# Kernel optimization log

Hardware: AMD Instinct MI355X
Metric: run time of the kernel (lower is better)

Reference implementation:

```python
import jax, jax.numpy as jnp
import numpy as np

B, S, DIM = 2, 2048, 2048
NH, NKV = 16, 16
HD = 128            # constructor head_dim (full per-head dim, = 2 * self.head_dim)
HHD = HD // 2       # self.head_dim = per-stream dim = 64
ROPE_THETA = 10000.0
LAMBDA_INIT = 0.8 - 0.6 * float(np.exp(-0.3 * 0))  # block_id = 0 -> 0.2
EPS = 1e-5


def make_freq_cis(seq_len, dim, theta):
    # rotation matrices, shape (seq, dim//2, 2, 2): [[cos, -sin], [sin, cos]]
    inv = 1.0 / (theta ** (np.arange(0, dim, 2, dtype=np.float32) / dim))
    ang = np.arange(seq_len, dtype=np.float32)[:, None] * inv[None, :]
    cos, sin = np.cos(ang), np.sin(ang)
    fc = np.stack([np.stack([cos, -sin], -1), np.stack([sin, cos], -1)], -2)
    return jnp.asarray(fc, dtype=jnp.float32)


def setup_inputs() -> dict:
    key = jax.random.key(0)
    ks = jax.random.split(key, 9)
    std = DIM ** -0.5
    return {
        "x": jax.random.normal(ks[0], (B, S, DIM), jnp.float32),
        "freq_cis": make_freq_cis(S, HD, ROPE_THETA),
        "wq": jax.random.normal(ks[1], (NH * HD, DIM), jnp.float32) * std,
        "wk": jax.random.normal(ks[2], (NKV * HD, DIM), jnp.float32) * std,
        "wv": jax.random.normal(ks[3], (NKV * HD, DIM), jnp.float32) * std,
        "wo": jax.random.normal(ks[4], (DIM, NH * HD), jnp.float32) * std,
        "lambda_q1": jax.random.normal(ks[5], (HHD,), jnp.float32) * 0.1,
        "lambda_k1": jax.random.normal(ks[6], (HHD,), jnp.float32) * 0.1,
        "lambda_q2": jax.random.normal(ks[7], (HHD,), jnp.float32) * 0.1,
        "lambda_k2": jax.random.normal(ks[8], (HHD,), jnp.float32) * 0.1,
        "subln_w": jnp.ones((HD,), jnp.float32),
    }


def _rope(t, fc):
    # t: (b, s, h, d); fc: (s, d//2, 2, 2). Pairs (even, odd) rotated by 2x2 matrix.
    b, s, h, d = t.shape
    t2 = t.reshape(b, s, h, d // 2, 1, 2)
    out = (t2 * fc[None, :, None]).sum(-1)  # (b, s, h, d//2, 2)
    return out.reshape(b, s, h, d)


def _causal_attn(q, k, v):
    # q, k: (b, s, h, HHD); v: (b, s, h, HD). Flash-attn default scale = 1/sqrt(q head dim).
    scale = 1.0 / jnp.sqrt(jnp.asarray(q.shape[-1], q.dtype))
    scores = jnp.einsum('bqhd,bkhd->bhqk', q, k) * scale
    s = q.shape[1]
    causal = jnp.tril(jnp.ones((s, s), bool))
    scores = jnp.where(causal, scores, jnp.finfo(scores.dtype).min)
    p = jax.nn.softmax(scores, axis=-1)
    return jnp.einsum('bhqk,bkhd->bqhd', p, v)  # (b, s, h, HD)


def reference(x, freq_cis, wq, wk, wv, wo, lambda_q1, lambda_k1, lambda_q2, lambda_k2, subln_w):
    b, s, _ = x.shape
    xq = (x @ wq.T).reshape(b, s, NH, HD)
    xk = (x @ wk.T).reshape(b, s, NKV, HD)
    xv = (x @ wv.T).reshape(b, s, NKV, HD)
    xq = _rope(xq, freq_cis)
    xk = _rope(xk, freq_cis)
    if NKV != NH:  # GQA: repeat kv heads group-wise
        rep = NH // NKV
        xk = jnp.repeat(xk, rep, axis=2)
        xv = jnp.repeat(xv, rep, axis=2)
    # split each head into two differential streams of size HHD
    xq = xq.reshape(b, s, NH, 2, HHD)
    xk = xk.reshape(b, s, NH, 2, HHD)
    attn1 = _causal_attn(xq[:, :, :, 0], xk[:, :, :, 0], xv)
    attn2 = _causal_attn(xq[:, :, :, 1], xk[:, :, :, 1], xv)
    lam1 = jnp.exp(jnp.sum(lambda_q1 * lambda_k1))
    lam2 = jnp.exp(jnp.sum(lambda_q2 * lambda_k2))
    lam_full = lam1 - lam2 + LAMBDA_INIT
    attn = attn1 - lam_full * attn2              # (b, s, h, HD)
    attn = jnp.transpose(attn, (0, 2, 1, 3))     # faithful to torch .transpose(1, 2)
    ms = jnp.mean(jnp.square(attn), axis=-1, keepdims=True)
    attn = attn * jax.lax.rsqrt(ms + EPS) * subln_w  # RMSNorm(2*HHD)
    attn = attn * (1.0 - LAMBDA_INIT)
    # faithful to original: reshape (b, h, s, HD) row-major into (b, s, h*HD)
    attn = attn.reshape(b, s, NH * HD)
    return attn @ wo.T
```

## Files before the change

kernel.cpp:

```cpp
#include <hip/hip_runtime.h>

typedef unsigned short u16;
typedef unsigned int   u32;
typedef __attribute__((ext_vector_type(8))) short s16x8;
typedef __attribute__((ext_vector_type(4))) float f32x4;
typedef __attribute__((ext_vector_type(4))) u32   u32x4;

constexpr int Bc = 2, Sc = 2048, DIMc = 2048, NHc = 16, HDc = 128, Tc = Bc * Sc;
constexpr float LAMBDA_INIT_C = 0.2f;

__device__ __forceinline__ u16 f2bf(float f) {
  union { float f; u32 u; } v; v.f = f;
  u32 r = v.u + 0x7fffu + ((v.u >> 16) & 1u);
  return (u16)(r >> 16);
}
__device__ __forceinline__ float bf2f(u16 b) {
  union { u32 u; float f; } v; v.u = ((u32)b) << 16;
  return v.f;
}
__device__ __forceinline__ f32x4 mfma16(s16x8 a, s16x8 b, f32x4 c) {
  return __builtin_amdgcn_mfma_f32_16x16x32_bf16(a, b, c, 0, 0, 0);
}

typedef const __attribute__((address_space(1))) u32 gq32;
typedef __attribute__((address_space(3))) u32 lq32;
__device__ __forceinline__ void cp16(const u16* g, u16* l) {
  __builtin_amdgcn_global_load_lds((gq32*)g, (lq32*)l, 16, 0, 0);
}

#define BAR()    asm volatile("s_barrier" ::: "memory")
#define LGKM(n)  asm volatile("s_waitcnt lgkmcnt(" #n ")" ::: "memory")
#define VMC(n)   asm volatile("s_waitcnt vmcnt(" #n ")" ::: "memory")
#define SCHED0() __builtin_amdgcn_sched_barrier(0)

__global__ void cvt_all_kernel(const float* __restrict__ x,
                               const float* __restrict__ wq, const float* __restrict__ wk,
                               const float* __restrict__ wv, const float* __restrict__ wo,
                               u16* __restrict__ xb, u16* __restrict__ wb) {
  const int i = blockIdx.x * 256 + threadIdx.x;
  constexpr int NX = Tc * DIMc / 4;
  constexpr int PW = DIMc * DIMc / 4;
  float4 v; uint2* dst;
  if (i < NX) {
    v = ((const float4*)x)[i];
    dst = ((uint2*)xb) + i;
  } else {
    const int j = i - NX;
    const int which = j >> 20;
    const int jj = j & (PW - 1);
    const float* src = which == 0 ? wq : which == 1 ? wk : which == 2 ? wv : wo;
    v = ((const float4*)src)[jj];
    dst = ((uint2*)wb) + j;
  }
  union { u16 u[4]; uint2 p; } o;
  o.u[0] = f2bf(v.x); o.u[1] = f2bf(v.y); o.u[2] = f2bf(v.z); o.u[3] = f2bf(v.w);
  *dst = o.p;
}

__global__ __launch_bounds__(512, 2) void gemm8p(const u16* __restrict__ A,
                                                 const u16* __restrict__ Bw,
                                                 u16* __restrict__ Cb) {
  constexpr int K = 2048, NT = K / 64;
  constexpr int AU = 128 * 64;
  constexpr int BU = 256 * 64;
  __shared__ __align__(16) u16 L[2 * AU + 3 * BU];

  const int tid  = threadIdx.x;
  const int lane = tid & 63, w = tid >> 6;
  const int wm = w >> 2, wn = w & 3;
  const int l15 = lane & 15, quad = lane >> 4;

  const int mt   = gridDim.y;
  const int nwg  = gridDim.x * mt;
  const int flat = blockIdx.x * mt + blockIdx.y;
  const int swz  = (flat & 7) * (nwg >> 3) + (flat >> 3);
  const int nbase = (swz / mt) * 256;
  const int mbase = (swz % mt) * 128;

  const u16* Ag = A  + (size_t)mbase * K;
  const u16* Bg = Bw + (size_t)nbase * K;

  u32 soffA[2], dlinA[2], soffB[4], dlinB[4];
#pragma unroll
  for (int l = 0; l < 2; l++) {
    const int n = l * 512 + tid;
    const int r = n >> 3;
    const u32 q = (u32)((n & 7) ^ (r & 7));
    soffA[l] = (u32)r * K + q * 8;
    dlinA[l] = (u32)n * 8;
  }
#pragma unroll
  for (int l = 0; l < 4; l++) {
    const int n = l * 512 + tid;
    const int r = n >> 3;
    const u32 q = (u32)((n & 7) ^ (r & 7));
    soffB[l] = (u32)r * K + q * 8;
    dlinB[l] = (u32)n * 8;
  }

  auto stA = [&](int kt, int ab) {
    u16* base = L + ab * AU;
#pragma unroll
    for (int l = 0; l < 2; l++)
      cp16(Ag + (size_t)kt * 64 + soffA[l], base + dlinA[l]);
  };
  auto stB = [&](int kt, int bb) {
    u16* base = L + 2 * AU + bb * BU;
#pragma unroll
    for (int l = 0; l < 4; l++)
      cp16(Bg + (size_t)kt * 64 + soffB[l], base + dlinB[l]);
  };

  const int aB  = (wm * 64 + l15) * 64;
  const int bB  = (wn * 64 + l15) * 64;
  const int xq0 = (quad ^ (l15 & 7)) << 3;

  f32x4 acc[4][4];
#pragma unroll
  for (int i = 0; i < 4; i++)
#pragma unroll
    for (int j = 0; j < 4; j++) acc[i][j] = (f32x4){0.f, 0.f, 0.f, 0.f};

  stB(0, 0); stA(0, 0); stB(1, 1);
  VMC(4);
  BAR();

  s16x8 a0[4], b0[4], a1[4], b1[4];
  int abR = 0, bbR = 0;

  for (int kt = 0; kt < NT; ++kt) {
    const int tgA = (kt + 1 < NT) ? kt + 1 : 0;
    const int tgB = (kt + 2 < NT) ? kt + 2 : 0;
    const int abW = abR ^ 1;
    const int bbW = (bbR + 2 >= 3) ? bbR - 1 : bbR + 2;

    const u16* Ab = L + abR * AU;
    const u16* Bb = L + 2 * AU + bbR * BU;

#pragma unroll
    for (int j = 0; j < 4; j++)
      b0[j] = *(const s16x8*)(Bb + bB + j * 1024 + xq0);
#pragma unroll
    for (int i = 0; i < 4; i++)
      a0[i] = *(const s16x8*)(Ab + aB + i * 1024 + xq0);
    SCHED0();
#pragma unroll
    for (int j = 0; j < 4; j++)
      b1[j] = *(const s16x8*)(Bb + bB + j * 1024 + (xq0 ^ 32));
#pragma unroll
    for (int i = 0; i < 4; i++)
      a1[i] = *(const s16x8*)(Ab + aB + i * 1024 + (xq0 ^ 32));
    SCHED0();
    stA(tgA, abW);
    stB(tgB, bbW);

    LGKM(8); SCHED0();
    __builtin_amdgcn_s_setprio(1);
#pragma unroll
    for (int i = 0; i < 4; i++)
#pragma unroll
      for (int j = 0; j < 4; j++) acc[i][j] = mfma16(a0[i], b0[j], acc[i][j]);
    __builtin_amdgcn_s_setprio(0);

    LGKM(0); SCHED0();
    __builtin_amdgcn_s_setprio(1);
#pragma unroll
    for (int i = 0; i < 4; i++)
#pragma unroll
      for (int j = 0; j < 4; j++) acc[i][j] = mfma16(a1[i], b1[j], acc[i][j]);
    __builtin_amdgcn_s_setprio(0);

    VMC(4);
    BAR();

    abR = abW;
    bbR = (bbR + 1 == 3) ? 0 : bbR + 1;
  }
  asm volatile("s_waitcnt vmcnt(0)" ::: "memory");

  const int which = nbase >> 11;
  const int ncol  = nbase & 2047;
  u16* Ob = Cb + (size_t)which * ((size_t)Tc * DIMc);
#pragma unroll
  for (int i = 0; i < 4; i++) {
    const int m0 = mbase + wm * 64 + i * 16 + quad * 4;
#pragma unroll
    for (int j = 0; j < 4; j++) {
      const int n0 = ncol + wn * 64 + j * 16 + l15;
#pragma unroll
      for (int r = 0; r < 4; r++)
        Ob[(size_t)(m0 + r) * 2048 + n0] = f2bf(acc[i][j][r]);
    }
  }
}

__global__ __launch_bounds__(256, 2) void gemm128o(const u16* __restrict__ A,
                                                   const u16* __restrict__ Bw,
                                                   float* __restrict__ Cf) {
  constexpr int K = 2048, NT = K / 64;
  constexpr int AU = 128 * 64;
  constexpr int BU = 128 * 64;
  __shared__ __align__(16) u16 L[2 * AU + 3 * BU];

  const int tid  = threadIdx.x;
  const int lane = tid & 63, w = tid >> 6;
  const int wm = w >> 1, wn = w & 1;
  const int l15 = lane & 15, quad = lane >> 4;

  const int mt   = gridDim.y;
  const int nwg  = gridDim.x * mt;
  const int flat = blockIdx.x * mt + blockIdx.y;
  const int swz  = (flat & 7) * (nwg >> 3) + (flat >> 3);
  const int nbase = (swz / mt) * 128;
  const int mbase = (swz % mt) * 128;

  const u16* Ag = A  + (size_t)mbase * K;
  const u16* Bg = Bw + (size_t)nbase * K;

  u32 soff[4], dlin[4];
#pragma unroll
  for (int l = 0; l < 4; l++) {
    const int n = l * 256 + tid;
    const int r = n >> 3;
    const u32 q = (u32)((n & 7) ^ (r & 7));
    soff[l] = (u32)r * K + q * 8;
    dlin[l] = (u32)n * 8;
  }

  auto stA = [&](int kt, int ab) {
    u16* base = L + ab * AU;
#pragma unroll
    for (int l = 0; l < 4; l++)
      cp16(Ag + (size_t)kt * 64 + soff[l], base + dlin[l]);
  };
  auto stB = [&](int kt, int bb) {
    u16* base = L + 2 * AU + bb * BU;
#pragma unroll
    for (int l = 0; l < 4; l++)
      cp16(Bg + (size_t)kt * 64 + soff[l], base + dlin[l]);
  };

  const int aB  = (wm * 64 + l15) * 64;
  const int bB  = (wn * 64 + l15) * 64;
  const int xq0 = (quad ^ (l15 & 7)) << 3;

  f32x4 acc[4][4];
#pragma unroll
  for (int i = 0; i < 4; i++)
#pragma unroll
    for (int j = 0; j < 4; j++) acc[i][j] = (f32x4){0.f, 0.f, 0.f, 0.f};

  stB(0, 0); stA(0, 0); stB(1, 1);
  VMC(4);
  BAR();

  s16x8 a0[4], b0[4], a1[4], b1[4];
  int abR = 0, bbR = 0;

  for (int kt = 0; kt < NT; ++kt) {
    const int tgA = (kt + 1 < NT) ? kt + 1 : 0;
    const int tgB = (kt + 2 < NT) ? kt + 2 : 0;
    const int abW = abR ^ 1;
    const int bbW = (bbR + 2 >= 3) ? bbR - 1 : bbR + 2;

    const u16* Ab = L + abR * AU;
    const u16* Bb = L + 2 * AU + bbR * BU;

#pragma unroll
    for (int j = 0; j < 4; j++)
      b0[j] = *(const s16x8*)(Bb + bB + j * 1024 + xq0);
#pragma unroll
    for (int i = 0; i < 4; i++)
      a0[i] = *(const s16x8*)(Ab + aB + i * 1024 + xq0);
    SCHED0();
#pragma unroll
    for (int j = 0; j < 4; j++)
      b1[j] = *(const s16x8*)(Bb + bB + j * 1024 + (xq0 ^ 32));
#pragma unroll
    for (int i = 0; i < 4; i++)
      a1[i] = *(const s16x8*)(Ab + aB + i * 1024 + (xq0 ^ 32));
    SCHED0();
    stA(tgA, abW);
    stB(tgB, bbW);

    LGKM(8); SCHED0();
    __builtin_amdgcn_s_setprio(1);
#pragma unroll
    for (int i = 0; i < 4; i++)
#pragma unroll
      for (int j = 0; j < 4; j++) acc[i][j] = mfma16(a0[i], b0[j], acc[i][j]);
    __builtin_amdgcn_s_setprio(0);

    LGKM(0); SCHED0();
    __builtin_amdgcn_s_setprio(1);
#pragma unroll
    for (int i = 0; i < 4; i++)
#pragma unroll
      for (int j = 0; j < 4; j++) acc[i][j] = mfma16(a1[i], b1[j], acc[i][j]);
    __builtin_amdgcn_s_setprio(0);

    VMC(4);
    BAR();

    abR = abW;
    bbR = (bbR + 1 == 3) ? 0 : bbR + 1;
  }
  asm volatile("s_waitcnt vmcnt(0)" ::: "memory");

#pragma unroll
  for (int i = 0; i < 4; i++) {
    const int m0 = mbase + wm * 64 + i * 16 + quad * 4;
#pragma unroll
    for (int j = 0; j < 4; j++) {
      const int n0 = nbase + wn * 64 + j * 16 + l15;
#pragma unroll
      for (int r = 0; r < 4; r++)
        Cf[(size_t)(m0 + r) * 2048 + n0] = acc[i][j][r];
    }
  }
}

__global__ void prep_kernel(const u16* __restrict__ qg, const u16* __restrict__ kg,
                            const u16* __restrict__ vg, const float* __restrict__ fc,
                            u16* __restrict__ qr, u16* __restrict__ kr,
                            u16* __restrict__ vt) {
  __shared__ u16 tile[64][33];
  const int bid = blockIdx.x;
  if (bid < 8192) {
    const bool isq = bid < 4096;
    const u16* xg = isq ? qg : kg;
    u16* outp = isq ? qr : kr;
    const float scale = isq ? 0.125f : 1.0f;
    const int idx = (bid & 4095) * 256 + threadIdx.x;
    const int p4 = idx & 15;
    const int hh = (idx >> 4) & 15;
    const int tt = idx >> 8;
    const int s  = tt & (Sc - 1);
    const int bb = tt >> 11;
    const u32x4 xp = *(const u32x4*)(xg + (size_t)tt * DIMc + hh * HDc + p4 * 8);
    u32x4 ow;
#pragma unroll
    for (int pp = 0; pp < 4; pp++) {
      const int p = p4 * 4 + pp;
      const float4 f = ((const float4*)fc)[s * 64 + p];
      const float c = f.x * scale, sn = f.z * scale;
      const u32 wd = xp[pp];
      const float x0 = bf2f((u16)wd), x1 = bf2f((u16)(wd >> 16));
      ow[pp] = (u32)f2bf(c * x0 - sn * x1) | ((u32)f2bf(sn * x0 + c * x1) << 16);
    }
    *(u32x4*)(outp + ((size_t)(bb * NHc + hh) * Sc + s) * HDc + p4 * 8) = ow;
  } else {
    const int vb = bid - 8192;
    const int bh = vb >> 7;
    const int bb = bh >> 4, hh = bh & 15;
    const int rem = vb & 127;
    const int s0 = (rem & 63) * 32, d0 = (rem >> 6) * 64;
    const int tx = threadIdx.x & 31, ty = threadIdx.x >> 5;
#pragma unroll
    for (int pp = 0; pp < 4; pp++) {
      const int s = s0 + ty + pp * 8;
      const u32 v = *(const u32*)(vg + (size_t)(bb * Sc + s) * DIMc + hh * HDc + d0 + tx * 2);
      tile[tx * 2][ty + pp * 8]     = (u16)v;
      tile[tx * 2 + 1][ty + pp * 8] = (u16)(v >> 16);
    }
    __syncthreads();
    const int dr = threadIdx.x >> 4;
    const int sx = threadIdx.x & 15;
#pragma unroll
    for (int pp = 0; pp < 4; pp++) {
      const int d = dr + pp * 16;
      const u32 wd = (u32)tile[d][sx * 2] | ((u32)tile[d][sx * 2 + 1] << 16);
      *(u32*)(vt + ((size_t)bh * HDc + d0 + d) * Sc + s0 + sx * 2) = wd;
    }
  }
}

__global__ __launch_bounds__(256, 3) void diff_attn_kernel(
    const u16* __restrict__ qr, const u16* __restrict__ kr, const u16* __restrict__ vt,
    const float* __restrict__ lq1, const float* __restrict__ lk1,
    const float* __restrict__ lq2, const float* __restrict__ lk2,
    const float* __restrict__ subw, u16* __restrict__ Y) {
  __shared__ u16 KB[2][8192];
  __shared__ u16 VB[2][8192];

  const int h = blockIdx.y, b = blockIdx.z;
  const int t = 31 - (int)blockIdx.x;
  const int bh = b * NHc + h;
  const int tid = threadIdx.x;
  const int w = tid >> 6, lane = tid & 63;
  const int l15 = lane & 15, quad = lane >> 4;

  const u16* krb = kr + (size_t)bh * Sc * HDc;
  const u16* vtb = vt + (size_t)bh * HDc * Sc;

  float lp1 = lq1[lane] * lk1[lane];
  float lp2 = lq2[lane] * lk2[lane];
#pragma unroll
  for (int m = 32; m; m >>= 1) { lp1 += __shfl_xor(lp1, m); lp2 += __shfl_xor(lp2, m); }
  const float lam = __expf(lp1) - __expf(lp2) + LAMBDA_INIT_C;

  float wsub[8];
#pragma unroll
  for (int dn = 0; dn < 8; dn++) wsub[dn] = subw[dn * 16 + l15];

  u32 offK[4], offV[4], dstO[4];
#pragma unroll
  for (int oo = 0; oo < 4; oo++) {
    const int n = w * 256 + oo * 64 + lane;
    const int s = n & 31, dblk = (n >> 5) & 15, sub = n >> 9;
    const int mkey = (s & 3) + ((s >> 2) & 3) * 8 + ((s >> 4) << 2);
    offK[oo] = (u32)((sub * 32 + mkey) * HDc + dblk * 8);
    offV[oo] = (u32)((n & 127) * Sc + (sub * 32 + ((n >> 7) & 3) * 8));
    dstO[oo] = (u32)(n * 8);
  }

  const int rowbase = t * 64 + w * 16;
  const int nc = t + 1;

  const u16* qp = qr + ((size_t)bh * Sc + rowbase + l15) * HDc + quad * 8;
  s16x8 qa[2][2];
  qa[0][0] = *(const s16x8*)(qp);
  qa[0][1] = *(const s16x8*)(qp + 32);
  qa[1][0] = *(const s16x8*)(qp + 64);
  qa[1][1] = *(const s16x8*)(qp + 96);

  f32x4 o[2][8];
#pragma unroll
  for (int st = 0; st < 2; st++)
#pragma unroll
    for (int dn = 0; dn < 8; dn++) o[st][dn] = (f32x4){0.f, 0.f, 0.f, 0.f};
  float lpart[2] = { 0.f, 0.f };

#pragma unroll
  for (int oo = 0; oo < 4; oo++) cp16(krb + offK[oo], KB[0] + dstO[oo]);
#pragma unroll
  for (int oo = 0; oo < 4; oo++) cp16(vtb + offV[oo], VB[0] + dstO[oo]);

  for (int c = 0; c < nc; c++) {
    __syncthreads();
    if (c + 1 < nc) {
      const int kb1 = (c + 1) * 64;
      u16* Kn = KB[(c + 1) & 1];
      u16* Vn = VB[(c + 1) & 1];
#pragma unroll
      for (int oo = 0; oo < 4; oo++) cp16(krb + (size_t)kb1 * HDc + offK[oo], Kn + dstO[oo]);
#pragma unroll
      for (int oo = 0; oo < 4; oo++) cp16(vtb + offV[oo] + kb1, Vn + dstO[oo]);
    }
    const u16* Kb = KB[c & 1];
    const u16* Vb = VB[c & 1];
    const int kb = c * 64;
    const bool diag = (c == nc - 1);

#pragma unroll
    for (int sub = 0; sub < 2; sub++) {
      if (diag && sub == 1 && w < 2) continue;

      f32x4 sc[2][2];
#pragma unroll
      for (int st = 0; st < 2; st++)
#pragma unroll
        for (int kt = 0; kt < 2; kt++) sc[st][kt] = (f32x4){0.f, 0.f, 0.f, 0.f};
#pragma unroll
      for (int st = 0; st < 2; st++)
#pragma unroll
        for (int kh = 0; kh < 2; kh++) {
          const int base = sub * 512 + (st * 8 + kh * 4 + quad) * 32;
#pragma unroll
          for (int kt = 0; kt < 2; kt++) {
            const s16x8 kf = *(const s16x8*)(Kb + (size_t)(base + kt * 16 + l15) * 8);
            sc[st][kt] = mfma16(kf, qa[st][kh], sc[st][kt]);
          }
        }

      s16x8 pa[2];
#pragma unroll
      for (int st = 0; st < 2; st++) {
        float p[8];
#pragma unroll
        for (int kt = 0; kt < 2; kt++)
#pragma unroll
          for (int r = 0; r < 4; r++) p[kt * 4 + r] = __expf(sc[st][kt][r]);
        if (diag) {
          const int qrow = rowbase + l15;
          const int kb0 = kb + sub * 32 + quad * 8;
#pragma unroll
          for (int j8 = 0; j8 < 8; j8++)
            if (kb0 + j8 > qrow) p[j8] = 0.f;
        }
        float sm = 0.f;
#pragma unroll
        for (int j8 = 0; j8 < 8; j8++) sm += p[j8];
        lpart[st] += sm;
        union { u16 us[8]; s16x8 vv; } pk;
#pragma unroll
        for (int j8 = 0; j8 < 8; j8++) pk.us[j8] = f2bf(p[j8]);
        pa[st] = pk.vv;
      }

#pragma unroll
      for (int dn = 0; dn < 8; dn++) {
        const s16x8 vf =
            *(const s16x8*)(Vb + (size_t)(sub * 512 + quad * 128 + dn * 16 + l15) * 8);
        o[0][dn] = mfma16(pa[0], vf, o[0][dn]);
        o[1][dn] = mfma16(pa[1], vf, o[1][dn]);
      }
    }
  }

  float lL0 = lpart[0], lL1 = lpart[1];
  lL0 += __shfl_xor(lL0, 16); lL0 += __shfl_xor(lL0, 32);
  lL1 += __shfl_xor(lL1, 16); lL1 += __shfl_xor(lL1, 32);
  const float inv1 = 1.f / lL0;
  const float inv2 = lam / lL1;
  float i1C[4], i2C[4];
#pragma unroll
  for (int r = 0; r < 4; r++) {
    i1C[r] = __shfl(inv1, quad * 4 + r, 16);
    i2C[r] = __shfl(inv2, quad * 4 + r, 16);
  }
  float yv[8][4], ss[4] = { 0.f, 0.f, 0.f, 0.f };
#pragma unroll
  for (int dn = 0; dn < 8; dn++)
#pragma unroll
    for (int r = 0; r < 4; r++) {
      const float y = o[0][dn][r] * i1C[r] - o[1][dn][r] * i2C[r];
      yv[dn][r] = y;
      ss[r] += y * y;
    }
#pragma unroll
  for (int r = 0; r < 4; r++) {
#pragma unroll
    for (int mm = 1; mm < 16; mm <<= 1) ss[r] += __shfl_xor(ss[r], mm);
  }
  float scl[4];
#pragma unroll
  for (int r = 0; r < 4; r++) scl[r] = rsqrtf(ss[r] * (1.f / 128.f) + 1e-5f) * 0.8f;

  u16* yrow = Y + ((size_t)(b * Sc + h * 128 + t * 4 + w)) * 2048;
#pragma unroll
  for (int dn = 0; dn < 8; dn++)
#pragma unroll
    for (int r = 0; r < 4; r++)
      yrow[(quad * 4 + r) * 128 + dn * 16 + l15] = f2bf(yv[dn][r] * scl[r] * wsub[dn]);
}

extern "C" void kernel_launch(void* const* d_in, const int* in_sizes, int n_in,
                              void* d_out, int out_size, void* d_ws, size_t ws_size,
                              hipStream_t stream) {
  const float* x    = (const float*)d_in[0];
  const float* fc   = (const float*)d_in[1];
  const float* wq   = (const float*)d_in[2];
  const float* wk   = (const float*)d_in[3];
  const float* wv   = (const float*)d_in[4];
  const float* wo   = (const float*)d_in[5];
  const float* lq1  = (const float*)d_in[6];
  const float* lk1  = (const float*)d_in[7];
  const float* lq2  = (const float*)d_in[8];
  const float* lk2  = (const float*)d_in[9];
  const float* subw = (const float*)d_in[10];
  float* out = (float*)d_out;

  char* ws = (char*)d_ws;
  constexpr size_t SZ_X  = (size_t)Tc * DIMc * 2;
  constexpr size_t SZ_W  = (size_t)DIMc * DIMc * 2;
  constexpr size_t SZ_T  = (size_t)Tc * DIMc * 2;
  u16* xb  = (u16*)(ws);
  u16* wqb = (u16*)(ws + SZ_X);
  u16* wob = (u16*)(ws + SZ_X + 3 * SZ_W);
  u16* qg  = (u16*)(ws + SZ_X + 4 * SZ_W);
  u16* kg  = (u16*)(ws + SZ_X + 4 * SZ_W + SZ_T);
  u16* vg  = (u16*)(ws + SZ_X + 4 * SZ_W + 2 * SZ_T);
  u16* qr  = (u16*)(ws + SZ_X + 4 * SZ_W + 3 * SZ_T);
  u16* kr  = (u16*)(ws + SZ_X + 4 * SZ_W + 4 * SZ_T);
  u16* vt  = (u16*)(ws + SZ_X + 4 * SZ_W + 5 * SZ_T);
  u16* Y   = (u16*)(ws + SZ_X + 4 * SZ_W + 6 * SZ_T);

  cvt_all_kernel<<<(Tc * DIMc / 4 + 4 * DIMc * DIMc / 4) / 256, 256, 0, stream>>>(
      x, wq, wk, wv, wo, xb, wqb);

  gemm8p<<<dim3(DIMc * 3 / 256, Tc / 128), 512, 0, stream>>>(xb, wqb, qg);

  prep_kernel<<<8192 + 4096, 256, 0, stream>>>(qg, kg, vg, fc, qr, kr, vt);

  diff_attn_kernel<<<dim3(32, NHc, Bc), 256, 0, stream>>>(
      qr, kr, vt, lq1, lk1, lq2, lk2, subw, Y);

  gemm128o<<<dim3(DIMc / 128, Tc / 128), 256, 0, stream>>>(Y, wob, out);
}
```

Before: 505.0 us.

## Merge two adjacent query tiles per 512-thread block sharing K/V loads

Each attention block now has 8 waves covering two consecutive 64-row query tiles, so every K/V chunk copied into shared memory serves 128 query rows and global/LDS load traffic per row is halved. Each thread issues half as many async copies per chunk. The lower tile's waves skip the last chunk but still hit the barriers, which leaves some idle wave time. The order of query tiles alternates by batch and block parity to balance causal work across the grid. Launch bounds change to 512 threads, which tightens the register budget per wave.

```diff
diff --git a/kernel.cpp b/kernel.cpp
--- a/kernel.cpp
+++ b/kernel.cpp
@@ -375,7 +375,7 @@
   }
 }
 
-__global__ __launch_bounds__(256, 3) void diff_attn_kernel(
+__global__ __launch_bounds__(512, 4) void diff_attn_kernel(
     const u16* __restrict__ qr, const u16* __restrict__ kr, const u16* __restrict__ vt,
     const float* __restrict__ lq1, const float* __restrict__ lk1,
     const float* __restrict__ lq2, const float* __restrict__ lk2,
@@ -384,12 +384,17 @@
   __shared__ u16 VB[2][8192];
 
   const int h = blockIdx.y, b = blockIdx.z;
-  const int t = 31 - (int)blockIdx.x;
+  const int bx = blockIdx.x;
+  const int uu = ((bx & 1) ^ b) ? (bx >> 1) : 15 - (bx >> 1);
   const int bh = b * NHc + h;
   const int tid = threadIdx.x;
   const int w = tid >> 6, lane = tid & 63;
   const int l15 = lane & 15, quad = lane >> 4;
 
+  const int tw = uu * 2 + (w >> 2);
+  const int rowbase = tw * 64 + (w & 3) * 16;
+  const int nc = uu * 2 + 2;
+
   const u16* krb = kr + (size_t)bh * Sc * HDc;
   const u16* vtb = vt + (size_t)bh * HDc * Sc;
 
@@ -403,19 +408,16 @@
 #pragma unroll
   for (int dn = 0; dn < 8; dn++) wsub[dn] = subw[dn * 16 + l15];
 
-  u32 offK[4], offV[4], dstO[4];
-#pragma unroll
-  for (int oo = 0; oo < 4; oo++) {
-    const int n = w * 256 + oo * 64 + lane;
+  u32 offK[2], offV[2], dstO[2];
+#pragma unroll
+  for (int l = 0; l < 2; l++) {
+    const int n = l * 512 + tid;
     const int s = n & 31, dblk = (n >> 5) & 15, sub = n >> 9;
     const int mkey = (s & 3) + ((s >> 2) & 3) * 8 + ((s >> 4) << 2);
-    offK[oo] = (u32)((sub * 32 + mkey) * HDc + dblk * 8);
-    offV[oo] = (u32)((n & 127) * Sc + (sub * 32 + ((n >> 7) & 3) * 8));
-    dstO[oo] = (u32)(n * 8);
-  }
-
-  const int rowbase = t * 64 + w * 16;
-  const int nc = t + 1;
+    offK[l] = (u32)((sub * 32 + mkey) * HDc + dblk * 8);
+    offV[l] = (u32)((n & 127) * Sc + (sub * 32 + ((n >> 7) & 3) * 8));
+    dstO[l] = (u32)(n * 8);
+  }
 
   const u16* qp = qr + ((size_t)bh * Sc + rowbase + l15) * HDc + quad * 8;
   s16x8 qa[2][2];
@@ -432,9 +434,9 @@
   float lpart[2] = { 0.f, 0.f };
 
 #pragma unroll
-  for (int oo = 0; oo < 4; oo++) cp16(krb + offK[oo], KB[0] + dstO[oo]);
-#pragma unroll
-  for (int oo = 0; oo < 4; oo++) cp16(vtb + offV[oo], VB[0] + dstO[oo]);
+  for (int l = 0; l < 2; l++) cp16(krb + offK[l], KB[0] + dstO[l]);
+#pragma unroll
+  for (int l = 0; l < 2; l++) cp16(vtb + offV[l], VB[0] + dstO[l]);
 
   for (int c = 0; c < nc; c++) {
     __syncthreads();
@@ -443,18 +445,19 @@
       u16* Kn = KB[(c + 1) & 1];
       u16* Vn = VB[(c + 1) & 1];
 #pragma unroll
-      for (int oo = 0; oo < 4; oo++) cp16(krb + (size_t)kb1 * HDc + offK[oo], Kn + dstO[oo]);
-#pragma unroll
-      for (int oo = 0; oo < 4; oo++) cp16(vtb + offV[oo] + kb1, Vn + dstO[oo]);
-    }
+      for (int l = 0; l < 2; l++) cp16(krb + (size_t)kb1 * HDc + offK[l], Kn + dstO[l]);
+#pragma unroll
+      for (int l = 0; l < 2; l++) cp16(vtb + offV[l] + kb1, Vn + dstO[l]);
+    }
+    if (c > tw) continue;
     const u16* Kb = KB[c & 1];
     const u16* Vb = VB[c & 1];
     const int kb = c * 64;
-    const bool diag = (c == nc - 1);
+    const bool diag = (c == tw);
 
 #pragma unroll
     for (int sub = 0; sub < 2; sub++) {
-      if (diag && sub == 1 && w < 2) continue;
+      if (diag && sub == 1 && (w & 3) < 2) continue;
 
       f32x4 sc[2][2];
 #pragma unroll
@@ -537,7 +540,7 @@
 #pragma unroll
   for (int r = 0; r < 4; r++) scl[r] = rsqrtf(ss[r] * (1.f / 128.f) + 1e-5f) * 0.8f;
 
-  u16* yrow = Y + ((size_t)(b * Sc + h * 128 + t * 4 + w)) * 2048;
+  u16* yrow = Y + ((size_t)(b * Sc + h * 128 + tw * 4 + (w & 3))) * 2048;
 #pragma unroll
   for (int dn = 0; dn < 8; dn++)
 #pragma unroll
@@ -583,7 +586,7 @@
 
   prep_kernel<<<8192 + 4096, 256, 0, stream>>>(qg, kg, vg, fc, qr, kr, vt);
 
-  diff_attn_kernel<<<dim3(32, NHc, Bc), 256, 0, stream>>>(
+  diff_attn_kernel<<<dim3(16, NHc, Bc), 512, 0, stream>>>(
       qr, kr, vt, lq1, lk1, lq2, lk2, subw, Y);
 
   gemm128o<<<dim3(DIMc / 128, Tc / 128), 256, 0, stream>>>(Y, wob, out);
```

New measurement: 424.6 us. 1.19x faster.
